# Performance work log

Hardware: AMD Instinct MI355X
Metric: run time of the kernel (lower is better)

## Reference

```python
import jax, jax.numpy as jnp
import numpy as np

N = 10000   # nodes
E = 320000  # directed edges (self-loops added inside reference, per PyG default)
H1, C = 4, 128  # gat1: 4 heads x 128; gat2: 1 head x 128
NEG_SLOPE = 0.2


def _glorot(k, shape):
    lim = float(np.sqrt(6.0 / (shape[0] + shape[-1])))
    return jax.random.uniform(k, shape, jnp.float32, -lim, lim)


def setup_inputs() -> dict:
    key = jax.random.key(0)
    ks = jax.random.split(key, 12)
    x = jax.random.normal(ks[0], (N, 2), jnp.float32)
    edge_index = jax.random.randint(ks[1], (2, E), 0, N, dtype=jnp.int32).astype(jnp.int64)
    W1 = _glorot(ks[2], (2, H1 * C))
    att_src1 = _glorot(ks[3], (H1, C))
    att_dst1 = _glorot(ks[4], (H1, C))
    b1 = jnp.zeros((H1 * C,), jnp.float32)
    W2 = _glorot(ks[5], (H1 * C, C))
    att_src2 = _glorot(ks[6], (1, C))
    att_dst2 = _glorot(ks[7], (1, C))
    b2 = jnp.zeros((C,), jnp.float32)
    Wp = _glorot(ks[8], (C, 1))
    bp = jnp.zeros((1,), jnp.float32)
    return dict(x=x, edge_index=edge_index, W1=W1, att_src1=att_src1, att_dst1=att_dst1,
                b1=b1, W2=W2, att_src2=att_src2, att_dst2=att_dst2, b2=b2, Wp=Wp, bp=bp)


def _gat_conv(x, src, dst, W, a_src, a_dst, b, heads, ch, concat):
    n = x.shape[0]
    h = (x @ W).reshape(n, heads, ch)                         # [N,H,C]
    # per-node attention halves, gathered per edge
    e = jax.nn.leaky_relu((h * a_src).sum(-1)[src] + (h * a_dst).sum(-1)[dst],
                          NEG_SLOPE)                           # [E,H]
    # segment softmax over incoming edges of each destination node
    m = jax.ops.segment_max(e, dst, num_segments=n)            # [N,H]
    p = jnp.exp(e - m[dst])
    s = jax.ops.segment_sum(p, dst, num_segments=n)
    alpha = p / (s[dst] + 1e-16)                               # [E,H]
    out = jax.ops.segment_sum(h[src] * alpha[..., None], dst, num_segments=n)  # [N,H,C]
    out = out.reshape(n, heads * ch) if concat else out.mean(axis=1)
    return out + b


def reference(x, edge_index, W1, att_src1, att_dst1, b1, W2, att_src2, att_dst2, b2, Wp, bp):
    n = x.shape[0]
    loop = jnp.arange(n, dtype=edge_index.dtype)               # PyG add_self_loops=True
    src = jnp.concatenate([edge_index[0], loop])
    dst = jnp.concatenate([edge_index[1], loop])
    h = jax.nn.relu(_gat_conv(x, src, dst, W1, att_src1, att_dst1, b1, H1, C, True))
    h = jax.nn.relu(_gat_conv(h, src, dst, W2, att_src2, att_dst2, b2, 1, C, True))
    logits = h @ Wp + bp                                       # [N,1]
    return logits.squeeze(-1)
```

## Files before the change

### kernel.cpp

```cpp
#include <hip/hip_runtime.h>
#include <hip/hip_fp16.h>
#include <math.h>

#define N_NODES 10000
#define E_IN    320000
#define E_TOT   330000
#define H1      4
#define C       128
#define F1      512

__global__ __launch_bounds__(256) void k_as1z(
    const float* __restrict__ x, const float* __restrict__ W1,
    const float* __restrict__ asw, const float* __restrict__ adw,
    float4* __restrict__ as1v, float4* __restrict__ ad1v, int* __restrict__ deg)
{
    __shared__ float red[4][8];
    __shared__ float prep_s[16];
    int tid = threadIdx.x;
    {
        int j = tid;
        int j2 = tid + 256;
        float w0a = W1[j],  w1a = W1[F1 + j];
        float w0b = W1[j2], w1b = W1[F1 + j2];
        float aa = asw[j], dd = adw[j], ab = asw[j2], db = adw[j2];
        float q0 = w0a*aa, q1 = w1a*aa, q2 = w0a*dd, q3 = w1a*dd;
        float q4 = w0b*ab, q5 = w1b*ab, q6 = w0b*db, q7 = w1b*db;
        #pragma unroll
        for (int o = 32; o > 0; o >>= 1) {
            q0 += __shfl_down(q0, o); q1 += __shfl_down(q1, o);
            q2 += __shfl_down(q2, o); q3 += __shfl_down(q3, o);
            q4 += __shfl_down(q4, o); q5 += __shfl_down(q5, o);
            q6 += __shfl_down(q6, o); q7 += __shfl_down(q7, o);
        }
        int wave = tid >> 6, lane = tid & 63;
        if (lane == 0) {
            red[wave][0] = q0; red[wave][1] = q1; red[wave][2] = q2; red[wave][3] = q3;
            red[wave][4] = q4; red[wave][5] = q5; red[wave][6] = q6; red[wave][7] = q7;
        }
        __syncthreads();
        if (tid < 16) {
            int t = tid >> 2;
            int h = tid & 3;
            int w0 = (h & 1) * 2;
            int r  = t + (h >> 1) * 4;
            prep_s[t*4 + h] = red[w0][r] + red[w0+1][r];
        }
        __syncthreads();
    }
    int n = blockIdx.x * 256 + tid;
    if (n >= N_NODES) return;
    deg[n] = 0;
    float x0 = x[2*n], x1 = x[2*n+1];
    float4 A0 = *(const float4*)(prep_s);
    float4 A1 = *(const float4*)(prep_s + 4);
    float4 D0 = *(const float4*)(prep_s + 8);
    float4 D1 = *(const float4*)(prep_s + 12);
    as1v[n] = make_float4(x0*A0.x + x1*A1.x, x0*A0.y + x1*A1.y,
                          x0*A0.z + x1*A1.z, x0*A0.w + x1*A1.w);
    ad1v[n] = make_float4(x0*D0.x + x1*D1.x, x0*D0.y + x1*D1.y,
                          x0*D0.z + x1*D1.z, x0*D0.w + x1*D1.w);
}

__global__ void k_hist(const int* __restrict__ dsti, int* __restrict__ deg) {
    int t = blockIdx.x * blockDim.x + threadIdx.x;
    if (t >= E_TOT) return;
    int d = (t < E_IN) ? dsti[t] : (t - E_IN);
    atomicAdd(&deg[d], 1);
}

__global__ __launch_bounds__(256) void k_scan(
    const int* __restrict__ deg, int* __restrict__ offs, int* __restrict__ cursor)
{
    __shared__ int part[256];
    int tid = threadIdx.x;
    const int CH = (N_NODES + 255) / 256;
    int start = tid * CH;
    int sum = 0;
    for (int i = 0; i < CH; ++i) { int idx = start + i; if (idx < N_NODES) sum += deg[idx]; }
    part[tid] = sum;
    __syncthreads();
    for (int off = 1; off < 256; off <<= 1) {
        int v = (tid >= off) ? part[tid - off] : 0;
        __syncthreads();
        part[tid] += v;
        __syncthreads();
    }
    int base = (tid == 0) ? 0 : part[tid - 1];
    for (int i = 0; i < CH; ++i) {
        int idx = start + i;
        if (idx < N_NODES) { offs[idx] = base; cursor[idx] = base; base += deg[idx]; }
    }
    if (tid == 255) offs[N_NODES] = base;
}

__global__ void k_scatter(const int* __restrict__ srci, const int* __restrict__ dsti,
                          int* __restrict__ cursor, int* __restrict__ scsr) {
    int t = blockIdx.x * blockDim.x + threadIdx.x;
    if (t >= E_TOT) return;
    int d = (t < E_IN) ? dsti[t] : (t - E_IN);
    int s = (t < E_IN) ? srci[t] : (t - E_IN);
    int pos = atomicAdd(&cursor[d], 1);
    scsr[pos] = s;
}

__global__ __launch_bounds__(256) void k_fused1(
    const int* __restrict__ offs, const int* __restrict__ scsr,
    const float4* __restrict__ as1v, const float4* __restrict__ ad1v,
    const float2* __restrict__ xv, float* __restrict__ wxn)
{
    int node = blockIdx.x * 16 + (threadIdx.x >> 4);
    int sub = threadIdx.x & 15;
    int beg = offs[node], end = offs[node + 1];
    float4 ad = ad1v[node];
    float s0 = 0.f, s1 = 0.f, s2 = 0.f, s3 = 0.f;
    float w00 = 0.f, w01 = 0.f, w10 = 0.f, w11 = 0.f;
    float w20 = 0.f, w21 = 0.f, w30 = 0.f, w31 = 0.f;
    for (int i = beg + sub; i < end; i += 16) {
        int s = scsr[i];
        float4 a = as1v[s];
        float2 xs = xv[s];
        float e0 = a.x + ad.x; e0 = e0 > 0.f ? e0 : 0.2f*e0;
        float e1 = a.y + ad.y; e1 = e1 > 0.f ? e1 : 0.2f*e1;
        float e2 = a.z + ad.z; e2 = e2 > 0.f ? e2 : 0.2f*e2;
        float e3 = a.w + ad.w; e3 = e3 > 0.f ? e3 : 0.2f*e3;
        float p0 = __expf(e0), p1 = __expf(e1), p2 = __expf(e2), p3 = __expf(e3);
        s0 += p0; s1 += p1; s2 += p2; s3 += p3;
        w00 += p0*xs.x; w01 += p0*xs.y; w10 += p1*xs.x; w11 += p1*xs.y;
        w20 += p2*xs.x; w21 += p2*xs.y; w30 += p3*xs.x; w31 += p3*xs.y;
    }
    #pragma unroll
    for (int o = 1; o < 16; o <<= 1) {
        s0 += __shfl_xor(s0, o); s1 += __shfl_xor(s1, o);
        s2 += __shfl_xor(s2, o); s3 += __shfl_xor(s3, o);
        w00 += __shfl_xor(w00, o); w01 += __shfl_xor(w01, o);
        w10 += __shfl_xor(w10, o); w11 += __shfl_xor(w11, o);
        w20 += __shfl_xor(w20, o); w21 += __shfl_xor(w21, o);
        w30 += __shfl_xor(w30, o); w31 += __shfl_xor(w31, o);
    }
    if (sub == 0) {
        float i0 = 1.f/(s0 + 1e-16f), i1 = 1.f/(s1 + 1e-16f);
        float i2 = 1.f/(s2 + 1e-16f), i3 = 1.f/(s3 + 1e-16f);
        float4* W = (float4*)(wxn + node*8);
        W[0] = make_float4(w00*i0, w01*i0, w10*i1, w11*i1);
        W[1] = make_float4(w20*i2, w21*i2, w30*i3, w31*i3);
    }
}

__global__ __launch_bounds__(256) void k_gemm2(
    const float* __restrict__ wxn, const float* __restrict__ W1,
    const float* __restrict__ b1, const float* __restrict__ W2,
    const float* __restrict__ asw, const float* __restrict__ adw,
    __half* __restrict__ h2h, float* __restrict__ as2, float* __restrict__ ad2)
{
    __shared__ float B_lds[64 * C];
    __shared__ float A_lds[64 * 16];
    __shared__ float wls[16 * 9];
    int tid = threadIdx.x;
    int n0 = blockIdx.x * 16;
    if (tid < 128) {
        int n = tid >> 3, q = tid & 7;
        wls[n*9 + q] = wxn[(n0 + n)*8 + q];
    }
    int cg = tid & 31;
    int ng = tid >> 5;
    int e_n = tid & 15, e_kq = tid >> 4;
    float acc00 = 0.f, acc01 = 0.f, acc02 = 0.f, acc03 = 0.f;
    float acc10 = 0.f, acc11 = 0.f, acc12 = 0.f, acc13 = 0.f;

    for (int kc = 0; kc < 8; ++kc) {
        __syncthreads();
        const float* Wsrc = W2 + kc * (64 * C);
        #pragma unroll
        for (int i = 0; i < 8; ++i)
            *(float4*)(B_lds + tid*4 + i*1024) = *(const float4*)(Wsrc + tid*4 + i*1024);
        int h2i = (kc >> 1) * 2;
        float wa = wls[e_n*9 + h2i], wb = wls[e_n*9 + h2i + 1];
        #pragma unroll
        for (int u = 0; u < 4; ++u) {
            int kl = e_kq*4 + u;
            int kg = kc*64 + kl;
            float v = wa * W1[kg] + wb * W1[F1 + kg] + b1[kg];
            A_lds[kl*16 + e_n] = v > 0.f ? v : 0.f;
        }
        __syncthreads();
        #pragma unroll 8
        for (int k = 0; k < 64; ++k) {
            float2 a = *(const float2*)(A_lds + k*16 + 2*ng);
            float4 b = *(const float4*)(B_lds + k*C + 4*cg);
            acc00 += a.x*b.x; acc01 += a.x*b.y; acc02 += a.x*b.z; acc03 += a.x*b.w;
            acc10 += a.y*b.x; acc11 += a.y*b.y; acc12 += a.y*b.z; acc13 += a.y*b.w;
        }
    }
    int r0 = n0 + 2*ng;
    {
        __half2 lo0 = __floats2half2_rn(acc00, acc01);
        __half2 hi0 = __floats2half2_rn(acc02, acc03);
        __half2 lo1 = __floats2half2_rn(acc10, acc11);
        __half2 hi1 = __floats2half2_rn(acc12, acc13);
        *(uint2*)(h2h + (size_t)r0*C + 4*cg)     = make_uint2(*(uint*)&lo0, *(uint*)&hi0);
        *(uint2*)(h2h + (size_t)(r0+1)*C + 4*cg) = make_uint2(*(uint*)&lo1, *(uint*)&hi1);
    }
    float4 av = *(const float4*)(asw + 4*cg);
    float4 dv = *(const float4*)(adw + 4*cg);
    float ps0 = acc00*av.x + acc01*av.y + acc02*av.z + acc03*av.w;
    float pd0 = acc00*dv.x + acc01*dv.y + acc02*dv.z + acc03*dv.w;
    float ps1 = acc10*av.x + acc11*av.y + acc12*av.z + acc13*av.w;
    float pd1 = acc10*dv.x + acc11*dv.y + acc12*dv.z + acc13*dv.w;
    #pragma unroll
    for (int o = 1; o < 32; o <<= 1) {
        ps0 += __shfl_xor(ps0, o); pd0 += __shfl_xor(pd0, o);
        ps1 += __shfl_xor(ps1, o); pd1 += __shfl_xor(pd1, o);
    }
    if (cg == 0) {
        as2[r0] = ps0;   ad2[r0] = pd0;
        as2[r0+1] = ps1; ad2[r0+1] = pd1;
    }
}

__global__ __launch_bounds__(64) void k_agg2(
    const int* __restrict__ offs, const int* __restrict__ scsr,
    const float* __restrict__ as2, const float* __restrict__ ad2,
    const __half* __restrict__ h2h, const float* __restrict__ b2,
    const float* __restrict__ Wp, const float* __restrict__ bp,
    float* __restrict__ out)
{
    int n = blockIdx.x, lane = threadIdx.x;
    int beg = offs[n], end = offs[n + 1];
    float adn = ad2[n];
    float accx = 0.f, accy = 0.f, psum = 0.f;
    for (int i = beg; i < end; ++i) {
        int s = scsr[i];
        float e = as2[s] + adn; e = e > 0.f ? e : 0.2f*e;
        float p = __expf(e);
        psum += p;
        __half2 hv = *(const __half2*)(h2h + (size_t)s*C + 2*lane);
        float2 f = __half22float2(hv);
        accx += p * f.x; accy += p * f.y;
    }
    float inv = 1.f / (psum + 1e-16f);
    float2 bb = *(const float2*)(b2 + 2*lane);
    float2 wp = *(const float2*)(Wp + 2*lane);
    float v0 = accx*inv + bb.x; v0 = v0 > 0.f ? v0 : 0.f;
    float v1 = accy*inv + bb.y; v1 = v1 > 0.f ? v1 : 0.f;
    float contrib = v0*wp.x + v1*wp.y;
    #pragma unroll
    for (int o = 1; o < 64; o <<= 1) contrib += __shfl_xor(contrib, o);
    if (lane == 0) out[n] = contrib + bp[0];
}

extern "C" void kernel_launch(void* const* d_in, const int* in_sizes, int n_in,
                              void* d_out, int out_size, void* d_ws, size_t ws_size,
                              hipStream_t stream)
{
    const float* x    = (const float*)d_in[0];
    const int*   ei   = (const int*)d_in[1];
    const int*   srci = ei;
    const int*   dsti = ei + E_IN;
    const float* W1   = (const float*)d_in[2];
    const float* as1w = (const float*)d_in[3];
    const float* ad1w = (const float*)d_in[4];
    const float* b1   = (const float*)d_in[5];
    const float* W2   = (const float*)d_in[6];
    const float* as2w = (const float*)d_in[7];
    const float* ad2w = (const float*)d_in[8];
    const float* b2   = (const float*)d_in[9];
    const float* Wp   = (const float*)d_in[10];
    const float* bp   = (const float*)d_in[11];
    float* out = (float*)d_out;

    char* ws = (char*)d_ws;
    size_t off = 0;
    auto alloc = [&](size_t bytes) -> char* {
        char* p = ws + off;
        off = (off + bytes + 255) & ~(size_t)255;
        return p;
    };
    float4* as1v   = (float4*)alloc((size_t)N_NODES * 16);
    float4* ad1v   = (float4*)alloc((size_t)N_NODES * 16);
    float*  wxn    = (float*)alloc((size_t)N_NODES * 8 * 4);
    __half* h2h    = (__half*)alloc((size_t)N_NODES * C * 2);
    float*  as2    = (float*)alloc((size_t)N_NODES * 4);
    float*  ad2    = (float*)alloc((size_t)N_NODES * 4);
    int*    deg    = (int*)alloc((size_t)N_NODES * 4);
    int*    offs   = (int*)alloc((size_t)(N_NODES + 1) * 4);
    int*    cursor = (int*)alloc((size_t)N_NODES * 4);
    int*    scsr   = (int*)alloc((size_t)E_TOT * 4);

    const int EB = 256;
    const int egrid = (E_TOT + EB - 1) / EB;
    const int ngrid = (N_NODES + 255) / 256;

    k_as1z<<<ngrid, 256, 0, stream>>>(x, W1, as1w, ad1w, as1v, ad1v, deg);
    k_hist<<<egrid, EB, 0, stream>>>(dsti, deg);
    k_scan<<<1, 256, 0, stream>>>(deg, offs, cursor);
    k_scatter<<<egrid, EB, 0, stream>>>(srci, dsti, cursor, scsr);
    k_fused1<<<N_NODES / 16, 256, 0, stream>>>(offs, scsr, as1v, ad1v,
                                               (const float2*)x, wxn);
    k_gemm2<<<N_NODES / 16, 256, 0, stream>>>(wxn, W1, b1, W2, as2w, ad2w, h2h, as2, ad2);
    k_agg2<<<N_NODES, 64, 0, stream>>>(offs, scsr, as2, ad2, h2h, b2, Wp, bp, out);
}
```

Measured before the change: 217.8 us.

## Use fp16 MFMA for layer-2 GEMM and batch edge loads in aggregation

```diff
diff --git a/kernel.cpp b/kernel.cpp
--- a/kernel.cpp
+++ b/kernel.cpp
@@ -8,6 +8,9 @@
 #define H1      4
 #define C       128
 #define F1      512
+
+typedef _Float16 f16x8 __attribute__((ext_vector_type(8)));
+typedef float    f32x4 __attribute__((ext_vector_type(4)));
 
 __global__ __launch_bounds__(256) void k_as1z(
     const float* __restrict__ x, const float* __restrict__ W1,
@@ -146,95 +149,144 @@
     }
 }
 
-__global__ __launch_bounds__(256) void k_gemm2(
+__global__ __launch_bounds__(256, 1) void k_gemm2(
     const float* __restrict__ wxn, const float* __restrict__ W1,
     const float* __restrict__ b1, const float* __restrict__ W2,
     const float* __restrict__ asw, const float* __restrict__ adw,
     __half* __restrict__ h2h, float* __restrict__ as2, float* __restrict__ ad2)
 {
-    __shared__ float B_lds[64 * C];
-    __shared__ float A_lds[64 * 16];
-    __shared__ float wls[16 * 9];
+    __shared__ _Float16 w2t[F1 * C];
     int tid = threadIdx.x;
-    int n0 = blockIdx.x * 16;
-    if (tid < 128) {
-        int n = tid >> 3, q = tid & 7;
-        wls[n*9 + q] = wxn[(n0 + n)*8 + q];
-    }
-    int cg = tid & 31;
-    int ng = tid >> 5;
-    int e_n = tid & 15, e_kq = tid >> 4;
-    float acc00 = 0.f, acc01 = 0.f, acc02 = 0.f, acc03 = 0.f;
-    float acc10 = 0.f, acc11 = 0.f, acc12 = 0.f, acc13 = 0.f;
-
-    for (int kc = 0; kc < 8; ++kc) {
-        __syncthreads();
-        const float* Wsrc = W2 + kc * (64 * C);
+    {
+        int c0 = (tid & 63) * 2;
+        int kh = tid >> 6;
+        int xr0 = (c0 & 7) << 3;
+        int xr1 = ((c0 + 1) & 7) << 3;
+        for (int kb = 0; kb < 128; kb += 8) {
+            int k0 = kh * 128 + kb;
+            f16x8 p0, p1;
+            #pragma unroll
+            for (int jj = 0; jj < 8; ++jj) {
+                float2 w = *(const float2*)(W2 + (k0 + jj) * C + c0);
+                p0[jj] = (_Float16)w.x;
+                p1[jj] = (_Float16)w.y;
+            }
+            *(f16x8*)(&w2t[c0 * F1 + (k0 ^ xr0)])       = p0;
+            *(f16x8*)(&w2t[(c0 + 1) * F1 + (k0 ^ xr1)]) = p1;
+        }
+    }
+    __syncthreads();
+
+    int wid = tid >> 6, lane = tid & 63;
+    int tile = blockIdx.x * 4 + wid;
+    if (tile >= N_NODES / 16) return;
+    int n0w = tile * 16;
+    int col = lane & 15;
+    int krow = (lane >> 4) * 8;
+    int qr4 = (lane >> 4) * 4;
+    int node = n0w + col;
+
+    float4 wv0 = *(const float4*)(wxn + node * 8);
+    float4 wv1 = *(const float4*)(wxn + node * 8 + 4);
+
+    f32x4 acc[8];
+    #pragma unroll
+    for (int mt = 0; mt < 8; ++mt) acc[mt] = (f32x4){0.f, 0.f, 0.f, 0.f};
+
+    int xr = (col & 7) << 3;
+    const float* W1r0 = W1;
+    const float* W1r1 = W1 + F1;
+
+    #pragma unroll
+    for (int h = 0; h < 4; ++h) {
+        float wa = (h == 0) ? wv0.x : (h == 1) ? wv0.z : (h == 2) ? wv1.x : wv1.z;
+        float wb = (h == 0) ? wv0.y : (h == 1) ? wv0.w : (h == 2) ? wv1.y : wv1.w;
         #pragma unroll
-        for (int i = 0; i < 8; ++i)
-            *(float4*)(B_lds + tid*4 + i*1024) = *(const float4*)(Wsrc + tid*4 + i*1024);
-        int h2i = (kc >> 1) * 2;
-        float wa = wls[e_n*9 + h2i], wb = wls[e_n*9 + h2i + 1];
-        #pragma unroll
-        for (int u = 0; u < 4; ++u) {
-            int kl = e_kq*4 + u;
-            int kg = kc*64 + kl;
-            float v = wa * W1[kg] + wb * W1[F1 + kg] + b1[kg];
-            A_lds[kl*16 + e_n] = v > 0.f ? v : 0.f;
-        }
-        __syncthreads();
-        #pragma unroll 8
-        for (int k = 0; k < 64; ++k) {
-            float2 a = *(const float2*)(A_lds + k*16 + 2*ng);
-            float4 b = *(const float4*)(B_lds + k*C + 4*cg);
-            acc00 += a.x*b.x; acc01 += a.x*b.y; acc02 += a.x*b.z; acc03 += a.x*b.w;
-            acc10 += a.y*b.x; acc11 += a.y*b.y; acc12 += a.y*b.z; acc13 += a.y*b.w;
-        }
-    }
-    int r0 = n0 + 2*ng;
-    {
-        __half2 lo0 = __floats2half2_rn(acc00, acc01);
-        __half2 hi0 = __floats2half2_rn(acc02, acc03);
-        __half2 lo1 = __floats2half2_rn(acc10, acc11);
-        __half2 hi1 = __floats2half2_rn(acc12, acc13);
-        *(uint2*)(h2h + (size_t)r0*C + 4*cg)     = make_uint2(*(uint*)&lo0, *(uint*)&hi0);
-        *(uint2*)(h2h + (size_t)(r0+1)*C + 4*cg) = make_uint2(*(uint*)&lo1, *(uint*)&hi1);
-    }
-    float4 av = *(const float4*)(asw + 4*cg);
-    float4 dv = *(const float4*)(adw + 4*cg);
-    float ps0 = acc00*av.x + acc01*av.y + acc02*av.z + acc03*av.w;
-    float pd0 = acc00*dv.x + acc01*dv.y + acc02*dv.z + acc03*dv.w;
-    float ps1 = acc10*av.x + acc11*av.y + acc12*av.z + acc13*av.w;
-    float pd1 = acc10*dv.x + acc11*dv.y + acc12*dv.z + acc13*dv.w;
-    #pragma unroll
-    for (int o = 1; o < 32; o <<= 1) {
-        ps0 += __shfl_xor(ps0, o); pd0 += __shfl_xor(pd0, o);
-        ps1 += __shfl_xor(ps1, o); pd1 += __shfl_xor(pd1, o);
-    }
-    if (cg == 0) {
-        as2[r0] = ps0;   ad2[r0] = pd0;
-        as2[r0+1] = ps1; ad2[r0+1] = pd1;
-    }
-}
-
-__global__ __launch_bounds__(64) void k_agg2(
+        for (int kq = 0; kq < 4; ++kq) {
+            int kc = h * 4 + kq;
+            int k0 = kc * 32 + krow;
+            float4 a0 = *(const float4*)(W1r0 + k0);
+            float4 a1 = *(const float4*)(W1r0 + k0 + 4);
+            float4 c0 = *(const float4*)(W1r1 + k0);
+            float4 c1 = *(const float4*)(W1r1 + k0 + 4);
+            float4 b0 = *(const float4*)(b1 + k0);
+            float4 b1v = *(const float4*)(b1 + k0 + 4);
+            f16x8 bf;
+            float v;
+            v = wa*a0.x + wb*c0.x + b0.x;  bf[0] = (_Float16)(v > 0.f ? v : 0.f);
+            v = wa*a0.y + wb*c0.y + b0.y;  bf[1] = (_Float16)(v > 0.f ? v : 0.f);
+            v = wa*a0.z + wb*c0.z + b0.z;  bf[2] = (_Float16)(v > 0.f ? v : 0.f);
+            v = wa*a0.w + wb*c0.w + b0.w;  bf[3] = (_Float16)(v > 0.f ? v : 0.f);
+            v = wa*a1.x + wb*c1.x + b1v.x; bf[4] = (_Float16)(v > 0.f ? v : 0.f);
+            v = wa*a1.y + wb*c1.y + b1v.y; bf[5] = (_Float16)(v > 0.f ? v : 0.f);
+            v = wa*a1.z + wb*c1.z + b1v.z; bf[6] = (_Float16)(v > 0.f ? v : 0.f);
+            v = wa*a1.w + wb*c1.w + b1v.w; bf[7] = (_Float16)(v > 0.f ? v : 0.f);
+            int kbase = col * F1 + (k0 ^ xr);
+            #pragma unroll
+            for (int mt = 0; mt < 8; ++mt) {
+                f16x8 af = *(const f16x8*)(&w2t[mt * 16 * F1 + kbase]);
+                acc[mt] = __builtin_amdgcn_mfma_f32_16x16x32_f16(af, bf, acc[mt], 0, 0, 0);
+            }
+        }
+    }
+
+    float ps = 0.f, pd = 0.f;
+    __half* hbase = h2h + (size_t)node * C + qr4;
+    #pragma unroll
+    for (int mt = 0; mt < 8; ++mt) {
+        f32x4 a = acc[mt];
+        __half2 lo = __floats2half2_rn(a[0], a[1]);
+        __half2 hi = __floats2half2_rn(a[2], a[3]);
+        uint2 u; u.x = *(uint*)&lo; u.y = *(uint*)&hi;
+        *(uint2*)(hbase + mt * 16) = u;
+        float4 av = *(const float4*)(asw + mt * 16 + qr4);
+        float4 dv = *(const float4*)(adw + mt * 16 + qr4);
+        ps += a[0]*av.x + a[1]*av.y + a[2]*av.z + a[3]*av.w;
+        pd += a[0]*dv.x + a[1]*dv.y + a[2]*dv.z + a[3]*dv.w;
+    }
+    ps += __shfl_xor(ps, 16); ps += __shfl_xor(ps, 32);
+    pd += __shfl_xor(pd, 16); pd += __shfl_xor(pd, 32);
+    if (lane < 16) { as2[n0w + lane] = ps; ad2[n0w + lane] = pd; }
+}
+
+__global__ __launch_bounds__(256) void k_agg2(
     const int* __restrict__ offs, const int* __restrict__ scsr,
     const float* __restrict__ as2, const float* __restrict__ ad2,
     const __half* __restrict__ h2h, const float* __restrict__ b2,
     const float* __restrict__ Wp, const float* __restrict__ bp,
     float* __restrict__ out)
 {
-    int n = blockIdx.x, lane = threadIdx.x;
+    int n = blockIdx.x * 4 + (threadIdx.x >> 6);
+    int lane = threadIdx.x & 63;
     int beg = offs[n], end = offs[n + 1];
     float adn = ad2[n];
     float accx = 0.f, accy = 0.f, psum = 0.f;
-    for (int i = beg; i < end; ++i) {
+    int i = beg;
+    for (; i + 4 <= end; i += 4) {
+        int s0 = scsr[i+0], s1 = scsr[i+1], s2 = scsr[i+2], s3 = scsr[i+3];
+        float e0 = as2[s0] + adn, e1 = as2[s1] + adn;
+        float e2 = as2[s2] + adn, e3 = as2[s3] + adn;
+        __half2 q0 = *(const __half2*)(h2h + (size_t)s0*C + 2*lane);
+        __half2 q1 = *(const __half2*)(h2h + (size_t)s1*C + 2*lane);
+        __half2 q2 = *(const __half2*)(h2h + (size_t)s2*C + 2*lane);
+        __half2 q3 = *(const __half2*)(h2h + (size_t)s3*C + 2*lane);
+        e0 = e0 > 0.f ? e0 : 0.2f*e0;  float p0 = __expf(e0);
+        e1 = e1 > 0.f ? e1 : 0.2f*e1;  float p1 = __expf(e1);
+        e2 = e2 > 0.f ? e2 : 0.2f*e2;  float p2 = __expf(e2);
+        e3 = e3 > 0.f ? e3 : 0.2f*e3;  float p3 = __expf(e3);
+        psum += (p0 + p1) + (p2 + p3);
+        float2 f0 = __half22float2(q0), f1 = __half22float2(q1);
+        float2 f2 = __half22float2(q2), f3 = __half22float2(q3);
+        accx += p0*f0.x + p1*f1.x + p2*f2.x + p3*f3.x;
+        accy += p0*f0.y + p1*f1.y + p2*f2.y + p3*f3.y;
+    }
+    for (; i < end; ++i) {
         int s = scsr[i];
         float e = as2[s] + adn; e = e > 0.f ? e : 0.2f*e;
         float p = __expf(e);
         psum += p;
-        __half2 hv = *(const __half2*)(h2h + (size_t)s*C + 2*lane);
-        float2 f = __half22float2(hv);
+        __half2 q = *(const __half2*)(h2h + (size_t)s*C + 2*lane);
+        float2 f = __half22float2(q);
         accx += p * f.x; accy += p * f.y;
     }
     float inv = 1.f / (psum + 1e-16f);
@@ -296,6 +348,7 @@
     k_scatter<<<egrid, EB, 0, stream>>>(srci, dsti, cursor, scsr);
     k_fused1<<<N_NODES / 16, 256, 0, stream>>>(offs, scsr, as1v, ad1v,
                                                (const float2*)x, wxn);
-    k_gemm2<<<N_NODES / 16, 256, 0, stream>>>(wxn, W1, b1, W2, as2w, ad2w, h2h, as2, ad2);
-    k_agg2<<<N_NODES, 64, 0, stream>>>(offs, scsr, as2, ad2, h2h, b2, Wp, bp, out);
-}
+    k_gemm2<<<(N_NODES/16 + 3) / 4, 256, 0, stream>>>(wxn, W1, b1, W2, as2w, ad2w,
+                                                      h2h, as2, ad2);
+    k_agg2<<<N_NODES / 4, 256, 0, stream>>>(offs, scsr, as2, ad2, h2h, b2, Wp, bp, out);
+}
```

Measured after the change: 188.8 us. -13.3%, faster.
